# Performance work log

Measured on AMD Instinct MI355X. Metric: run time of the kernel, lower is better.

The kernel has to match this reference:

```python
import jax, jax.numpy as jnp
import numpy as np

B, N, D_IN, D_OUT = 4, 4096, 512, 256
ALPHA = 0.2          # LeakyReLU negative slope
NEG_BIG = -9e15      # value used to mask non-edges before softmax


def setup_inputs() -> dict:
    key = jax.random.key(0)
    k_h, k_adj, k_w, k_a = jax.random.split(key, 4)
    h = jax.random.normal(k_h, (B, N, D_IN), dtype=jnp.float32)
    adj = jax.random.randint(k_adj, (N, N), 0, 2, dtype=jnp.int32)
    # xavier_uniform with gain 1.414
    lim_w = 1.414 * np.sqrt(6.0 / (D_IN + D_OUT))
    Ws = jax.random.uniform(k_w, (B, D_IN, D_OUT), jnp.float32, -lim_w, lim_w)
    lim_a = 1.414 * np.sqrt(6.0 / (2 * D_OUT + 1))
    a = jax.random.uniform(k_a, (B, 2 * D_OUT, 1), jnp.float32, -lim_a, lim_a)
    return {"h": h, "adj": adj, "Ws": Ws, "a": a}


def reference(h, adj, Ws, a):
    d_out = Ws.shape[-1]
    Wh = jnp.einsum('bni,bio->bno', h, Ws)                 # [B,N,D_OUT]
    a1 = a[:, :d_out, 0]                                    # [B,D_OUT]
    a2 = a[:, d_out:, 0]                                    # [B,D_OUT]
    e1 = jnp.einsum('bno,bo->bn', Wh, a1)                   # [B,N]
    e2 = jnp.einsum('bno,bo->bn', Wh, a2)                   # [B,N]
    e = e1[:, :, None] + e2[:, None, :]                     # [B,N,N]
    e = jnp.where(e > 0, e, ALPHA * e)                      # LeakyReLU
    scores = jnp.where(adj[None, :, :] > 0, e, NEG_BIG)     # mask non-edges
    att = jax.nn.softmax(scores, axis=-1)                   # over neighbors j
    # dropout omitted (eval mode / p irrelevant for correctness baseline)
    h_prime = jnp.einsum('bnm,bmo->bno', att, Wh)           # [B,N,D_OUT]
    return jax.nn.elu(h_prime)                              # concat=True -> elu
```

## Files before the change

### kernel.cpp

```cpp
#include <hip/hip_runtime.h>
#include <hip/hip_bf16.h>
#include <stdint.h>

#define B_    4
#define NN    4096
#define DIN   512
#define DOUT  256
#define ALPHA_ 0.2f

typedef __attribute__((ext_vector_type(8))) short short8;
typedef __attribute__((ext_vector_type(4))) float f32x4;

typedef const __attribute__((address_space(1))) void gconst_void;
typedef __attribute__((address_space(3))) void lds_void;

__device__ __forceinline__ unsigned short f2bf(float x) {
    union { float f; uint32_t u; } v; v.f = x;
    uint32_t r = v.u + 0x7FFFu + ((v.u >> 16) & 1u);
    return (unsigned short)(r >> 16);
}
__device__ __forceinline__ float bf2f(unsigned short u) {
    union { uint32_t u; float f; } v; v.u = ((uint32_t)u) << 16;
    return v.f;
}

__global__ __launch_bounds__(256) void k_prep(const int* __restrict__ adj,
                                              const float4* __restrict__ h4,
                                              const float* __restrict__ Ws,
                                              uint32_t* __restrict__ bits,
                                              uint2* __restrict__ hb,
                                              unsigned short* __restrict__ wst) {
    const int gid = blockIdx.x;
    const int tid = threadIdx.x;
    if (gid < 65536) {
        int idx = gid * 256 + tid;
        unsigned long long m = __ballot(adj[idx] > 0);
        if ((tid & 63) == 0)
            *reinterpret_cast<unsigned long long*>(bits + ((idx >> 6) << 1)) = m;
    } else if (gid < 73728) {
        int idx = (gid - 65536) * 256 + tid;
        float4 v = h4[idx];
        uint2 o;
        o.x = (uint32_t)f2bf(v.x) | ((uint32_t)f2bf(v.y) << 16);
        o.y = (uint32_t)f2bf(v.z) | ((uint32_t)f2bf(v.w) << 16);
        hb[idx] = o;
    } else {
        int idx = (gid - 73728) * 256 + tid;
        int k = idx & (DIN - 1);
        int o = (idx >> 9) & (DOUT - 1);
        int b = idx >> 17;
        wst[idx] = f2bf(Ws[((size_t)b * DIN + k) * DOUT + o]);
    }
}

__global__ __launch_bounds__(256) void k_gemm1(const unsigned short* __restrict__ hb,
                                               const unsigned short* __restrict__ wst,
                                               const float* __restrict__ a,
                                               unsigned short* __restrict__ wht,
                                               float* __restrict__ e1,
                                               float* __restrict__ e2) {
    __shared__ unsigned short Ah[64 * 64];
    __shared__ unsigned short Bw[256 * 64];
    __shared__ float e1s[64], e2s[64];
    const int tid = threadIdx.x;
    const int w = tid >> 6, lane = tid & 63;
    const int l15 = lane & 15, lhi = lane >> 4;
    const int b = blockIdx.y;
    const int n0 = blockIdx.x * 64;
    const unsigned short* hrow = hb + ((size_t)b * NN + n0) * DIN;
    const unsigned short* wrow = wst + (size_t)b * DOUT * DIN;

    if (tid < 64) { e1s[tid] = 0.f; e2s[tid] = 0.f; }

    f32x4 acc[4][4] = {};

    for (int kt = 0; kt < DIN / 64; ++kt) {
        const int k0 = kt * 64;
        #pragma unroll
        for (int it = 0; it < 2; ++it) {
            int q = it * 256 + tid;
            int row = q >> 3, c = q & 7;
            const unsigned short* src = hrow + (size_t)row * DIN + k0 + 8 * (c ^ (row & 7));
            char* dst = reinterpret_cast<char*>(Ah) + it * 4096 + w * 1024;
            __builtin_amdgcn_global_load_lds((gconst_void*)src, (lds_void*)dst, 16, 0, 0);
        }
        #pragma unroll
        for (int it = 0; it < 8; ++it) {
            int q = it * 256 + tid;
            int row = q >> 3, c = q & 7;
            const unsigned short* src = wrow + (size_t)row * DIN + k0 + 8 * (c ^ (row & 7));
            char* dst = reinterpret_cast<char*>(Bw) + it * 4096 + w * 1024;
            __builtin_amdgcn_global_load_lds((gconst_void*)src, (lds_void*)dst, 16, 0, 0);
        }
        __syncthreads();
        #pragma unroll
        for (int kk = 0; kk < 2; ++kk) {
            short8 af[4], bfr[4];
            #pragma unroll
            for (int rf = 0; rf < 4; ++rf) {
                int row = rf * 16 + l15;
                int off = row * 128 + ((kk * 64 + lhi * 16) ^ ((row & 7) << 4));
                af[rf] = *reinterpret_cast<const short8*>(reinterpret_cast<const char*>(Ah) + off);
            }
            #pragma unroll
            for (int cf = 0; cf < 4; ++cf) {
                int row = w * 64 + cf * 16 + l15;
                int off = row * 128 + ((kk * 64 + lhi * 16) ^ ((row & 7) << 4));
                bfr[cf] = *reinterpret_cast<const short8*>(reinterpret_cast<const char*>(Bw) + off);
            }
            #pragma unroll
            for (int rf = 0; rf < 4; ++rf)
                #pragma unroll
                for (int cf = 0; cf < 4; ++cf)
                    acc[rf][cf] = __builtin_amdgcn_mfma_f32_16x16x32_bf16(af[rf], bfr[cf], acc[rf][cf], 0, 0, 0);
        }
        __syncthreads();
    }
    unsigned short* wb = wht + (size_t)b * DOUT * NN;
    #pragma unroll
    for (int rf = 0; rf < 4; ++rf) {
        #pragma unroll
        for (int cf = 0; cf < 4; ++cf) {
            int d = w * 64 + cf * 16 + l15;
            int m = n0 + rf * 16 + lhi * 4;
            uint2 pk;
            pk.x = (uint32_t)f2bf(acc[rf][cf][0]) | ((uint32_t)f2bf(acc[rf][cf][1]) << 16);
            pk.y = (uint32_t)f2bf(acc[rf][cf][2]) | ((uint32_t)f2bf(acc[rf][cf][3]) << 16);
            *reinterpret_cast<uint2*>(wb + (size_t)d * NN + m) = pk;
        }
    }
    const float* ab = a + b * 2 * DOUT;
    float a1v[4], a2v[4];
    #pragma unroll
    for (int cf = 0; cf < 4; ++cf) {
        int d = w * 64 + cf * 16 + l15;
        a1v[cf] = ab[d];
        a2v[cf] = ab[DOUT + d];
    }
    #pragma unroll
    for (int rf = 0; rf < 4; ++rf) {
        #pragma unroll
        for (int j = 0; j < 4; ++j) {
            float p1 = 0.f, p2 = 0.f;
            #pragma unroll
            for (int cf = 0; cf < 4; ++cf) {
                p1 = fmaf(acc[rf][cf][j], a1v[cf], p1);
                p2 = fmaf(acc[rf][cf][j], a2v[cf], p2);
            }
            #pragma unroll
            for (int msk = 1; msk < 16; msk <<= 1) {
                p1 += __shfl_xor(p1, msk);
                p2 += __shfl_xor(p2, msk);
            }
            if (l15 == 0) {
                atomicAdd(&e1s[rf * 16 + lhi * 4 + j], p1);
                atomicAdd(&e2s[rf * 16 + lhi * 4 + j], p2);
            }
        }
    }
    __syncthreads();
    if (tid < 64) {
        e1[b * NN + n0 + tid] = e1s[tid];
        e2[b * NN + n0 + tid] = e2s[tid];
    }
}

__global__ __launch_bounds__(256, 2) void k_attn(const unsigned short* __restrict__ wht,
                                                 const uint32_t* __restrict__ bits,
                                                 const float* __restrict__ e1,
                                                 const float* __restrict__ e2,
                                                 float* __restrict__ out) {
    __shared__ unsigned short Bw[2 * 256 * 64];
    __shared__ unsigned short Pt[2 * 32 * 64];
    __shared__ float sums[32];

    const int tid = threadIdx.x;
    const int w = tid >> 6, lane = tid & 63;
    const int l15 = lane & 15, lhi = lane >> 4;

    const int bid = blockIdx.x;
    const int wg = ((bid & 7) << 6) | (bid >> 3);
    const int b  = wg >> 7;
    const int n0 = (wg & 127) << 5;

    const int pr = tid >> 3, pc = tid & 7;
    const int gn = n0 + pr;
    const float r1 = e1[b * NN + gn];
    const float r2 = ALPHA_ * r1;
    const uint8_t* browb = reinterpret_cast<const uint8_t*>(bits) + (size_t)gn * (NN / 8);
    const float* e2g = e2 + b * NN;
    const unsigned short* wb = wht + (size_t)b * DOUT * NN;

    f32x4 acc[2][4] = {};
    float psum = 0.f;

    #pragma unroll
    for (int it = 0; it < 8; ++it) {
        int q = it * 256 + tid;
        int row = q >> 3, c = q & 7;
        const unsigned short* src = wb + (size_t)row * NN + 8 * (c ^ (row & 7));
        char* dst = reinterpret_cast<char*>(Bw) + it * 4096 + w * 1024;
        __builtin_amdgcn_global_load_lds((gconst_void*)src, (lds_void*)dst, 16, 0, 0);
    }
    {
        uint32_t bb = browb[pc];
        const float4* ep = reinterpret_cast<const float4*>(e2g + pc * 8);
        float4 ea = ep[0], eb = ep[1];
        float pv[8] = {ea.x, ea.y, ea.z, ea.w, eb.x, eb.y, eb.z, eb.w};
        #pragma unroll
        for (int j = 0; j < 8; ++j) {
            float s = r1 + pv[j];
            float t = fmaf(ALPHA_, pv[j], r2);
            float p = __expf(fmaxf(s, t));
            uint32_t msk = (uint32_t)(((int32_t)(bb << (31 - j))) >> 31);
            union { float f; uint32_t u; } pu; pu.f = p; pu.u &= msk;
            pv[j] = pu.f;
            psum += pv[j];
        }
        union { short8 v; uint32_t u[4]; } k0;
        #pragma unroll
        for (int i = 0; i < 4; ++i) {
            union { __hip_bfloat162 h; uint32_t u; } c0;
            c0.h = __float22bfloat162_rn(float2{pv[2 * i], pv[2 * i + 1]});
            k0.u[i] = c0.u;
        }
        *reinterpret_cast<short8*>(reinterpret_cast<char*>(Pt) + pr * 128 +
                                   ((pc * 16) ^ ((pr & 7) << 4))) = k0.v;
    }
    __syncthreads();

    #pragma unroll 2
    for (int t = 0; t < NN / 64; ++t) {
        const int cur = t & 1;
        uint32_t bbN = 0;
        float4 ea, eb;
        if (t < NN / 64 - 1) {
            const int m1 = (t + 1) * 64;
            #pragma unroll
            for (int it = 0; it < 8; ++it) {
                int q = it * 256 + tid;
                int row = q >> 3, c = q & 7;
                const unsigned short* src = wb + (size_t)row * NN + m1 + 8 * (c ^ (row & 7));
                char* dst = reinterpret_cast<char*>(Bw) + (cur ^ 1) * 32768 + it * 4096 + w * 1024;
                __builtin_amdgcn_global_load_lds((gconst_void*)src, (lds_void*)dst, 16, 0, 0);
            }
            bbN = browb[(m1 >> 3) + pc];
            const float4* ep = reinterpret_cast<const float4*>(e2g + m1 + pc * 8);
            ea = ep[0]; eb = ep[1];
        }
        __builtin_amdgcn_s_setprio(1);
        #pragma unroll
        for (int kk = 0; kk < 2; ++kk) {
            short8 af[2], bfr[4];
            #pragma unroll
            for (int rf = 0; rf < 2; ++rf) {
                int row = rf * 16 + l15;
                int off = row * 128 + ((kk * 64 + lhi * 16) ^ ((row & 7) << 4));
                af[rf] = *reinterpret_cast<const short8*>(
                    reinterpret_cast<const char*>(Pt) + cur * 4096 + off);
            }
            #pragma unroll
            for (int cf = 0; cf < 4; ++cf) {
                int row = w * 64 + cf * 16 + l15;
                int off = row * 128 + ((kk * 64 + lhi * 16) ^ ((row & 7) << 4));
                bfr[cf] = *reinterpret_cast<const short8*>(
                    reinterpret_cast<const char*>(Bw) + cur * 32768 + off);
            }
            #pragma unroll
            for (int rf = 0; rf < 2; ++rf)
                #pragma unroll
                for (int cf = 0; cf < 4; ++cf)
                    acc[rf][cf] = __builtin_amdgcn_mfma_f32_16x16x32_bf16(af[rf], bfr[cf], acc[rf][cf], 0, 0, 0);
        }
        __builtin_amdgcn_s_setprio(0);
        if (t < NN / 64 - 1) {
            float pv[8] = {ea.x, ea.y, ea.z, ea.w, eb.x, eb.y, eb.z, eb.w};
            #pragma unroll
            for (int j = 0; j < 8; ++j) {
                float s = r1 + pv[j];
                float tt = fmaf(ALPHA_, pv[j], r2);
                float p = __expf(fmaxf(s, tt));
                uint32_t msk = (uint32_t)(((int32_t)(bbN << (31 - j))) >> 31);
                union { float f; uint32_t u; } pu; pu.f = p; pu.u &= msk;
                pv[j] = pu.f;
                psum += pv[j];
            }
            union { short8 v; uint32_t u[4]; } k0;
            #pragma unroll
            for (int i = 0; i < 4; ++i) {
                union { __hip_bfloat162 h; uint32_t u; } c0;
                c0.h = __float22bfloat162_rn(float2{pv[2 * i], pv[2 * i + 1]});
                k0.u[i] = c0.u;
            }
            *reinterpret_cast<short8*>(reinterpret_cast<char*>(Pt) + (cur ^ 1) * 4096 + pr * 128 +
                                       ((pc * 16) ^ ((pr & 7) << 4))) = k0.v;
            __syncthreads();
        }
    }
    psum += __shfl_xor(psum, 1);
    psum += __shfl_xor(psum, 2);
    psum += __shfl_xor(psum, 4);
    if ((tid & 7) == 0) sums[pr] = psum;
    __syncthreads();
    #pragma unroll
    for (int rf = 0; rf < 2; ++rf) {
        #pragma unroll
        for (int cf = 0; cf < 4; ++cf) {
            int d = w * 64 + cf * 16 + l15;
            #pragma unroll
            for (int j = 0; j < 4; ++j) {
                int lr = rf * 16 + lhi * 4 + j;
                float x = acc[rf][cf][j] / sums[lr];
                x = x > 0.f ? x : (__expf(x) - 1.f);
                out[((size_t)b * NN + n0 + lr) * DOUT + d] = x;
            }
        }
    }
}

extern "C" void kernel_launch(void* const* d_in, const int* in_sizes, int n_in,
                              void* d_out, int out_size, void* d_ws, size_t ws_size,
                              hipStream_t stream) {
    (void)in_sizes; (void)n_in; (void)out_size; (void)ws_size;
    const float* h   = (const float*)d_in[0];
    const int*   adj = (const int*)d_in[1];
    const float* Ws  = (const float*)d_in[2];
    const float* a   = (const float*)d_in[3];
    float* out = (float*)d_out;

    char* ws = (char*)d_ws;
    unsigned short* hb  = (unsigned short*)(ws);
    unsigned short* wst = (unsigned short*)(ws + 16777216);
    unsigned short* wht = (unsigned short*)(ws + 17825792);
    float* e1  = (float*)(ws + 26214400);
    float* e2  = (float*)(ws + 26279936);
    uint32_t* bits = (uint32_t*)(ws + 26476544);

    k_prep<<<dim3(75776), dim3(256), 0, stream>>>(adj, (const float4*)h, Ws,
                                                  bits, (uint2*)hb, wst);
    k_gemm1<<<dim3(NN / 64, B_), dim3(256), 0, stream>>>(hb, wst, a, wht, e1, e2);
    k_attn<<<dim3(512), dim3(256), 0, stream>>>(wht, bits, e1, e2, out);
}
```

Baseline: 131.2 us.

## Retile attention kernel to 64 rows x 128 cols, compute P in registers

Each workgroup now covers 64 node rows and half of the output columns (128), with waves split 2x2, instead of 32 rows by all 256 columns. Each wave builds its own attention-probability A fragments directly in registers, which removes the shared P tile and one LDS round trip. Row sums come from an extra MFMA against a ones vector rather than shuffles and a shared array. The cost is that each exp/mask is computed twice (once per column half) and extra MFMA work is spent on the sums, while the LDS footprint per workgroup halves.

```diff
diff --git a/kernel.cpp b/kernel.cpp
--- a/kernel.cpp
+++ b/kernel.cpp
@@ -18,10 +18,6 @@
     union { float f; uint32_t u; } v; v.f = x;
     uint32_t r = v.u + 0x7FFFu + ((v.u >> 16) & 1u);
     return (unsigned short)(r >> 16);
-}
-__device__ __forceinline__ float bf2f(unsigned short u) {
-    union { uint32_t u; float f; } v; v.u = ((uint32_t)u) << 16;
-    return v.f;
 }
 
 __global__ __launch_bounds__(256) void k_prep(const int* __restrict__ adj,
@@ -170,149 +166,153 @@
                                                  const float* __restrict__ e1,
                                                  const float* __restrict__ e2,
                                                  float* __restrict__ out) {
-    __shared__ unsigned short Bw[2 * 256 * 64];
-    __shared__ unsigned short Pt[2 * 32 * 64];
-    __shared__ float sums[32];
+    __shared__ unsigned short Bw[2 * 128 * 64];
 
     const int tid = threadIdx.x;
     const int w = tid >> 6, lane = tid & 63;
-    const int l15 = lane & 15, lhi = lane >> 4;
+    const int l15 = lane & 15, lh4 = lane >> 4;
+    const int wn = w >> 1, wd = w & 1;
 
     const int bid = blockIdx.x;
     const int wg = ((bid & 7) << 6) | (bid >> 3);
     const int b  = wg >> 7;
-    const int n0 = (wg & 127) << 5;
-
-    const int pr = tid >> 3, pc = tid & 7;
-    const int gn = n0 + pr;
-    const float r1 = e1[b * NN + gn];
-    const float r2 = ALPHA_ * r1;
-    const uint8_t* browb = reinterpret_cast<const uint8_t*>(bits) + (size_t)gn * (NN / 8);
+    const int r  = wg & 127;
+    const int d0 = (r & 1) << 7;
+    const int n0 = (r >> 1) << 6;
+
+    const int gn = n0 + wn * 32 + l15;
+    const float r1a = e1[b * NN + gn];
+    const float r1b = e1[b * NN + gn + 16];
+    const float r2a = ALPHA_ * r1a, r2b = ALPHA_ * r1b;
+    const unsigned long long* bra =
+        reinterpret_cast<const unsigned long long*>(bits + (size_t)gn * (NN / 32));
+    const unsigned long long* brb =
+        reinterpret_cast<const unsigned long long*>(bits + (size_t)(gn + 16) * (NN / 32));
     const float* e2g = e2 + b * NN;
     const unsigned short* wb = wht + (size_t)b * DOUT * NN;
 
     f32x4 acc[2][4] = {};
-    float psum = 0.f;
-
-    #pragma unroll
-    for (int it = 0; it < 8; ++it) {
-        int q = it * 256 + tid;
-        int row = q >> 3, c = q & 7;
-        const unsigned short* src = wb + (size_t)row * NN + 8 * (c ^ (row & 7));
-        char* dst = reinterpret_cast<char*>(Bw) + it * 4096 + w * 1024;
-        __builtin_amdgcn_global_load_lds((gconst_void*)src, (lds_void*)dst, 16, 0, 0);
-    }
+    f32x4 accs[2] = {};
+    short8 ones;
     {
-        uint32_t bb = browb[pc];
-        const float4* ep = reinterpret_cast<const float4*>(e2g + pc * 8);
-        float4 ea = ep[0], eb = ep[1];
-        float pv[8] = {ea.x, ea.y, ea.z, ea.w, eb.x, eb.y, eb.z, eb.w};
-        #pragma unroll
-        for (int j = 0; j < 8; ++j) {
-            float s = r1 + pv[j];
-            float t = fmaf(ALPHA_, pv[j], r2);
-            float p = __expf(fmaxf(s, t));
-            uint32_t msk = (uint32_t)(((int32_t)(bb << (31 - j))) >> 31);
-            union { float f; uint32_t u; } pu; pu.f = p; pu.u &= msk;
-            pv[j] = pu.f;
-            psum += pv[j];
-        }
-        union { short8 v; uint32_t u[4]; } k0;
-        #pragma unroll
-        for (int i = 0; i < 4; ++i) {
-            union { __hip_bfloat162 h; uint32_t u; } c0;
-            c0.h = __float22bfloat162_rn(float2{pv[2 * i], pv[2 * i + 1]});
-            k0.u[i] = c0.u;
-        }
-        *reinterpret_cast<short8*>(reinterpret_cast<char*>(Pt) + pr * 128 +
-                                   ((pc * 16) ^ ((pr & 7) << 4))) = k0.v;
-    }
+        union { short8 v; uint32_t u[4]; } ov;
+        ov.u[0] = 0x3F803F80u; ov.u[1] = 0x3F803F80u;
+        ov.u[2] = 0x3F803F80u; ov.u[3] = 0x3F803F80u;
+        ones = ov.v;
+    }
+    short8 afA[2][2], afB[2][2];
+
+#define STAGE(T, BUF)                                                                  \
+    {                                                                                  \
+        _Pragma("unroll")                                                              \
+        for (int it = 0; it < 4; ++it) {                                               \
+            int q = it * 256 + tid;                                                    \
+            int row = q >> 3, c = q & 7;                                               \
+            const unsigned short* src =                                                \
+                wb + (size_t)(d0 + row) * NN + (T) * 64 + 8 * (c ^ (row & 7));         \
+            char* dst = reinterpret_cast<char*>(Bw) + (BUF) * 16384 + it * 4096 + w * 1024; \
+            __builtin_amdgcn_global_load_lds((gconst_void*)src, (lds_void*)dst, 16, 0, 0);  \
+        }                                                                              \
+    }
+
+#define P_COMPUTE(T, AFN)                                                              \
+    {                                                                                  \
+        unsigned long long bu0 = bra[T], bu1 = brb[T];                                 \
+        _Pragma("unroll")                                                              \
+        for (int kk = 0; kk < 2; ++kk) {                                               \
+            const float4* ep = reinterpret_cast<const float4*>(e2g + (T) * 64 + kk * 32 + lh4 * 8); \
+            float4 ea = ep[0], eb = ep[1];                                             \
+            float ev[8] = {ea.x, ea.y, ea.z, ea.w, eb.x, eb.y, eb.z, eb.w};            \
+            uint32_t bt0 = (uint32_t)(bu0 >> ((kk * 4 + lh4) * 8)) & 0xffu;            \
+            uint32_t bt1 = (uint32_t)(bu1 >> ((kk * 4 + lh4) * 8)) & 0xffu;            \
+            float p0[8], p1[8];                                                        \
+            _Pragma("unroll")                                                          \
+            for (int j = 0; j < 8; ++j) {                                              \
+                float e = ev[j];                                                       \
+                float s0 = r1a + e, q0 = fmaf(ALPHA_, e, r2a);                         \
+                float s1 = r1b + e, q1 = fmaf(ALPHA_, e, r2b);                         \
+                float x0 = __expf(fmaxf(s0, q0));                                      \
+                float x1 = __expf(fmaxf(s1, q1));                                      \
+                uint32_t m0 = (uint32_t)(((int32_t)(bt0 << (31 - j))) >> 31);          \
+                uint32_t m1 = (uint32_t)(((int32_t)(bt1 << (31 - j))) >> 31);          \
+                union { float f; uint32_t u; } u0, u1;                                 \
+                u0.f = x0; u0.u &= m0; u1.f = x1; u1.u &= m1;                          \
+                p0[j] = u0.f; p1[j] = u1.f;                                            \
+            }                                                                          \
+            union { short8 v; uint32_t u[4]; } k0, k1;                                 \
+            _Pragma("unroll")                                                          \
+            for (int i = 0; i < 4; ++i) {                                              \
+                union { __hip_bfloat162 h; uint32_t u; } c0, c1;                       \
+                c0.h = __float22bfloat162_rn(float2{p0[2 * i], p0[2 * i + 1]});        \
+                c1.h = __float22bfloat162_rn(float2{p1[2 * i], p1[2 * i + 1]});        \
+                k0.u[i] = c0.u; k1.u[i] = c1.u;                                        \
+            }                                                                          \
+            AFN[0][kk] = k0.v; AFN[1][kk] = k1.v;                                      \
+        }                                                                              \
+    }
+
+#define MM(T, AF)                                                                      \
+    {                                                                                  \
+        const char* base = reinterpret_cast<const char*>(Bw) + ((T) & 1) * 16384;      \
+        __builtin_amdgcn_s_setprio(1);                                                 \
+        _Pragma("unroll")                                                              \
+        for (int kk = 0; kk < 2; ++kk) {                                               \
+            short8 bf[4];                                                              \
+            _Pragma("unroll")                                                          \
+            for (int cf = 0; cf < 4; ++cf) {                                           \
+                int row = wd * 64 + cf * 16 + l15;                                     \
+                int off = row * 128 + ((kk * 64 + lh4 * 16) ^ ((row & 7) << 4));       \
+                bf[cf] = *reinterpret_cast<const short8*>(base + off);                 \
+            }                                                                          \
+            _Pragma("unroll")                                                          \
+            for (int rf = 0; rf < 2; ++rf) {                                           \
+                _Pragma("unroll")                                                      \
+                for (int cf = 0; cf < 4; ++cf)                                         \
+                    acc[rf][cf] = __builtin_amdgcn_mfma_f32_16x16x32_bf16(             \
+                        AF[rf][kk], bf[cf], acc[rf][cf], 0, 0, 0);                     \
+                accs[rf] = __builtin_amdgcn_mfma_f32_16x16x32_bf16(                    \
+                    AF[rf][kk], ones, accs[rf], 0, 0, 0);                              \
+            }                                                                          \
+        }                                                                              \
+        __builtin_amdgcn_s_setprio(0);                                                 \
+    }
+
+    STAGE(0, 0)
+    P_COMPUTE(0, afA)
     __syncthreads();
 
-    #pragma unroll 2
-    for (int t = 0; t < NN / 64; ++t) {
-        const int cur = t & 1;
-        uint32_t bbN = 0;
-        float4 ea, eb;
-        if (t < NN / 64 - 1) {
-            const int m1 = (t + 1) * 64;
-            #pragma unroll
-            for (int it = 0; it < 8; ++it) {
-                int q = it * 256 + tid;
-                int row = q >> 3, c = q & 7;
-                const unsigned short* src = wb + (size_t)row * NN + m1 + 8 * (c ^ (row & 7));
-                char* dst = reinterpret_cast<char*>(Bw) + (cur ^ 1) * 32768 + it * 4096 + w * 1024;
-                __builtin_amdgcn_global_load_lds((gconst_void*)src, (lds_void*)dst, 16, 0, 0);
-            }
-            bbN = browb[(m1 >> 3) + pc];
-            const float4* ep = reinterpret_cast<const float4*>(e2g + m1 + pc * 8);
-            ea = ep[0]; eb = ep[1];
-        }
-        __builtin_amdgcn_s_setprio(1);
-        #pragma unroll
-        for (int kk = 0; kk < 2; ++kk) {
-            short8 af[2], bfr[4];
-            #pragma unroll
-            for (int rf = 0; rf < 2; ++rf) {
-                int row = rf * 16 + l15;
-                int off = row * 128 + ((kk * 64 + lhi * 16) ^ ((row & 7) << 4));
-                af[rf] = *reinterpret_cast<const short8*>(
-                    reinterpret_cast<const char*>(Pt) + cur * 4096 + off);
-            }
-            #pragma unroll
-            for (int cf = 0; cf < 4; ++cf) {
-                int row = w * 64 + cf * 16 + l15;
-                int off = row * 128 + ((kk * 64 + lhi * 16) ^ ((row & 7) << 4));
-                bfr[cf] = *reinterpret_cast<const short8*>(
-                    reinterpret_cast<const char*>(Bw) + cur * 32768 + off);
-            }
-            #pragma unroll
-            for (int rf = 0; rf < 2; ++rf)
-                #pragma unroll
-                for (int cf = 0; cf < 4; ++cf)
-                    acc[rf][cf] = __builtin_amdgcn_mfma_f32_16x16x32_bf16(af[rf], bfr[cf], acc[rf][cf], 0, 0, 0);
-        }
-        __builtin_amdgcn_s_setprio(0);
-        if (t < NN / 64 - 1) {
-            float pv[8] = {ea.x, ea.y, ea.z, ea.w, eb.x, eb.y, eb.z, eb.w};
-            #pragma unroll
-            for (int j = 0; j < 8; ++j) {
-                float s = r1 + pv[j];
-                float tt = fmaf(ALPHA_, pv[j], r2);
-                float p = __expf(fmaxf(s, tt));
-                uint32_t msk = (uint32_t)(((int32_t)(bbN << (31 - j))) >> 31);
-                union { float f; uint32_t u; } pu; pu.f = p; pu.u &= msk;
-                pv[j] = pu.f;
-                psum += pv[j];
-            }
-            union { short8 v; uint32_t u[4]; } k0;
-            #pragma unroll
-            for (int i = 0; i < 4; ++i) {
-                union { __hip_bfloat162 h; uint32_t u; } c0;
-                c0.h = __float22bfloat162_rn(float2{pv[2 * i], pv[2 * i + 1]});
-                k0.u[i] = c0.u;
-            }
-            *reinterpret_cast<short8*>(reinterpret_cast<char*>(Pt) + (cur ^ 1) * 4096 + pr * 128 +
-                                       ((pc * 16) ^ ((pr & 7) << 4))) = k0.v;
-            __syncthreads();
-        }
-    }
-    psum += __shfl_xor(psum, 1);
-    psum += __shfl_xor(psum, 2);
-    psum += __shfl_xor(psum, 4);
-    if ((tid & 7) == 0) sums[pr] = psum;
-    __syncthreads();
+    for (int t = 0; t < NN / 64; t += 2) {
+        STAGE(t + 1, 1)
+        MM(t, afA)
+        P_COMPUTE(t + 1, afB)
+        __syncthreads();
+        if (t + 2 < NN / 64) {
+            STAGE(t + 2, 0)
+            MM(t + 1, afB)
+            P_COMPUTE(t + 2, afA)
+        } else {
+            MM(t + 1, afB)
+        }
+        __syncthreads();
+    }
+#undef STAGE
+#undef P_COMPUTE
+#undef MM
+
     #pragma unroll
     for (int rf = 0; rf < 2; ++rf) {
+        float inv[4];
+        #pragma unroll
+        for (int j = 0; j < 4; ++j) inv[j] = 1.0f / accs[rf][j];
         #pragma unroll
         for (int cf = 0; cf < 4; ++cf) {
-            int d = w * 64 + cf * 16 + l15;
+            int d = d0 + wd * 64 + cf * 16 + l15;
             #pragma unroll
             for (int j = 0; j < 4; ++j) {
-                int lr = rf * 16 + lhi * 4 + j;
-                float x = acc[rf][cf][j] / sums[lr];
+                int nr = n0 + wn * 32 + rf * 16 + lh4 * 4 + j;
+                float x = acc[rf][cf][j] * inv[j];
                 x = x > 0.f ? x : (__expf(x) - 1.f);
-                out[((size_t)b * NN + n0 + lr) * DOUT + d] = x;
+                out[((size_t)b * NN + nr) * DOUT + d] = x;
             }
         }
     }
```

Result: slower. 174.1 us (+32.7%).
